# Kernel optimization log

Hardware: AMD Instinct MI355X
Metric: run time of the kernel (lower is better)

## Reference

```python
import jax, jax.numpy as jnp
import numpy as np

NUM_NODES = 100000
NUM_EDGES = 3_200_000
WALKS_PER_NODE = 4
WALK_LENGTH = 8
SKIP_FIRST = True


def setup_inputs() -> dict:
    key = jax.random.key(0)
    k1, k2, k3 = jax.random.split(key, 3)
    edge_index = jax.random.randint(k1, (2, NUM_EDGES), 0, NUM_NODES, dtype=jnp.int32)
    edge_weight = jax.random.uniform(k2, (NUM_EDGES,), dtype=jnp.float32)
    # one uniform per walker per step; S = NUM_NODES * WALKS_PER_NODE
    rand_unif = jax.random.uniform(k3, (NUM_NODES * WALKS_PER_NODE, WALK_LENGTH), dtype=jnp.float32)
    return {"edge_index": edge_index, "edge_weight": edge_weight, "rand_unif": rand_unif}


def _random_walk_edges(edge_index, rand_unif):
    """Returns added [2, S*L] edges (root -> walked node), int dtype."""
    row, col = edge_index[0], edge_index[1]
    # is_sorted=False path: sort edges by source to build CSR
    order = jnp.argsort(row)
    row_s = row[order]
    col_s = col[order]
    deg = jax.ops.segment_sum(jnp.ones_like(row_s), row_s, num_segments=NUM_NODES)  # [N]
    rowptr = jnp.concatenate([jnp.zeros((1,), deg.dtype), jnp.cumsum(deg)])  # [N+1]
    # start = all nodes, repeated walks_per_node times
    start = jnp.tile(jnp.arange(NUM_NODES, dtype=row.dtype), WALKS_PER_NODE)  # [S]

    def step(cur, u):
        d = deg[cur]  # [S]
        off = jnp.minimum((u * d.astype(u.dtype)).astype(cur.dtype), jnp.maximum(d - 1, 0))
        nxt = jnp.where(d > 0, col_s[rowptr[cur] + off], cur)  # stay if isolated
        return nxt, nxt

    _, walks = jax.lax.scan(step, start, rand_unif.T)  # [L_total, S]
    walks = walks.T  # [S, WALK_LENGTH] == n_id[:, 1:]
    k = 1 if SKIP_FIRST else 0  # skip_first drops the first-hop node (n_id[:, 2:])
    targets = walks[:, k:]  # [S, L]
    L = targets.shape[1]
    roots = jnp.broadcast_to(start[:, None], (start.shape[0], L))
    return jnp.stack([roots.reshape(-1), targets.reshape(-1)])  # [2, S*L]


def reference(edge_index, edge_weight, rand_unif):
    added = _random_walk_edges(edge_index, rand_unif)
    out_edge_index = jnp.concatenate([edge_index, added], axis=1)
    added_w = jnp.ones((added.shape[1],), edge_weight.dtype)
    out_edge_weight = jnp.concatenate([edge_weight, added_w])
    return out_edge_index, out_edge_weight
```

## Files before the change

### kernel.cpp

```cpp
#include <hip/hip_runtime.h>

#define ARW_N_NODES   100000
#define ARW_N_EDGES   3200000
#define ARW_N_WALKERS 400000
#define ARW_WLEN      8
#define ARW_LOUT      7
#define ARW_ROW_LEN   6000000
#define ARW_OUT_ELEMS 18000000

#define ARW_NB    196
#define ARW_NT    3125
#define ARW_TP    3136
#define ARW_TILE  1024

#define ARW_HT    0
#define ARW_BT    700000
#define ARW_TOT   1350000
#define ARW_CB    1360000
#define ARW_DEG   1400000
#define ARW_RP    1500000
#define ARW_P     6000000
#define ARW_COLS  12000000

__global__ void AddRandomWalkEdge_16896401342869_kernel() {}

__global__ __launch_bounds__(1024) void arw16896_thist(const int* __restrict__ row,
                                                       int* __restrict__ s) {
    __shared__ int h[256];
    int tid = threadIdx.x;
    if (tid < 256) h[tid] = 0;
    __syncthreads();
    atomicAdd(&h[row[blockIdx.x * ARW_TILE + tid] >> 9], 1);
    __syncthreads();
    if (tid < ARW_NB) s[ARW_HT + tid * ARW_TP + blockIdx.x] = h[tid];
}

__global__ __launch_bounds__(1024) void arw16896_btot(int* __restrict__ s) {
    __shared__ int wsum[16];
    int b = blockIdx.x, tid = threadIdx.x, lane = tid & 63, wid = tid >> 6;
    int acc = 0;
    for (int t = tid; t < ARW_NT; t += 1024) acc += s[ARW_HT + b * ARW_TP + t];
    #pragma unroll
    for (int off = 32; off > 0; off >>= 1) acc += __shfl_down(acc, off, 64);
    if (lane == 0) wsum[wid] = acc;
    __syncthreads();
    if (tid == 0) {
        int a = 0;
        #pragma unroll
        for (int w = 0; w < 16; w++) a += wsum[w];
        s[ARW_TOT + b] = a;
    }
}

__global__ __launch_bounds__(256) void arw16896_bbase(int* __restrict__ s) {
    __shared__ int sm[256];
    int tid = threadIdx.x;
    int v = (tid < ARW_NB) ? s[ARW_TOT + tid] : 0;
    sm[tid] = v;
    __syncthreads();
    for (int off = 1; off < 256; off <<= 1) {
        int x = 0;
        if (tid >= off) x = sm[tid - off];
        __syncthreads();
        sm[tid] += x;
        __syncthreads();
    }
    if (tid < ARW_NB) s[ARW_CB + tid] = sm[tid] - v;
}

__global__ __launch_bounds__(1024) void arw16896_bscan2(int* __restrict__ s) {
    __shared__ int wsum[16];
    int b = blockIdx.x, tid = threadIdx.x, lane = tid & 63, wid = tid >> 6;
    int carry = s[ARW_CB + b];
    for (int c0 = 0; c0 < ARW_NT; c0 += 1024) {
        int t = c0 + tid;
        int v = (t < ARW_NT) ? s[ARW_HT + b * ARW_TP + t] : 0;
        int sv = v;
        #pragma unroll
        for (int off = 1; off < 64; off <<= 1) {
            int x = __shfl_up(sv, off, 64);
            if (lane >= off) sv += x;
        }
        if (lane == 63) wsum[wid] = sv;
        __syncthreads();
        int pre = 0, tot = 0;
        #pragma unroll
        for (int w = 0; w < 16; w++) {
            int x = wsum[w];
            if (w < wid) pre += x;
            tot += x;
        }
        if (t < ARW_NT) s[ARW_BT + b * ARW_TP + t] = carry + pre + sv - v;
        carry += tot;
        __syncthreads();
    }
}

__global__ __launch_bounds__(1024) void arw16896_part(const int* __restrict__ row,
                                                      const int* __restrict__ col,
                                                      int* __restrict__ s) {
    __shared__ unsigned W[16 * 256];
    int tid  = threadIdx.x;
    int wave = tid >> 6, lane = tid & 63;
    int e = blockIdx.x * ARW_TILE + tid;
    int r = row[e], cv = col[e];
    int b = r >> 9;
    W[tid] = 0; W[tid + 1024] = 0; W[tid + 2048] = 0; W[tid + 3072] = 0;
    __syncthreads();
    unsigned long long mask = ~0ULL;
    #pragma unroll
    for (int bit = 0; bit < 8; bit++) {
        unsigned long long bal = __ballot((b >> bit) & 1);
        mask &= ((b >> bit) & 1) ? bal : ~bal;
    }
    int rankw = __popcll(mask & ((1ULL << lane) - 1ULL));
    W[wave * 256 + b] = (unsigned)__popcll(mask);
    __syncthreads();
    int cross = 0;
    for (int w2 = 0; w2 < 16; w2++) {
        if (w2 >= wave) break;
        cross += (int)W[w2 * 256 + b];
    }
    int base = s[ARW_BT + b * ARW_TP + blockIdx.x];
    s[ARW_P + base + cross + rankw] = ((r & 511) << 17) | cv;
}

__global__ __launch_bounds__(1024) void arw16896_pass2(int* __restrict__ s) {
    __shared__ unsigned W[16 * 512];
    __shared__ int hist[512], pref[512], runc[512];
    int tid = threadIdx.x, lane = tid & 63, wave = tid >> 6;
    int b = blockIdx.x;
    int start = s[ARW_BT + b * ARW_TP];
    int end   = (b == ARW_NB - 1) ? ARW_N_EDGES : s[ARW_BT + (b + 1) * ARW_TP];
    int cnt = end - start;
    int rows0 = b << 9;
    int nrows = ARW_N_NODES - rows0; if (nrows > 512) nrows = 512;

    if (tid < 512) hist[tid] = 0;
    __syncthreads();
    for (int k = tid; k < cnt; k += 1024)
        atomicAdd(&hist[(unsigned)s[ARW_P + start + k] >> 17], 1);
    __syncthreads();
    if (tid < 512) pref[tid] = hist[tid];
    __syncthreads();
    for (int off = 1; off < 512; off <<= 1) {
        int x = 0;
        if (tid < 512 && tid >= off) x = pref[tid - off];
        __syncthreads();
        if (tid < 512) pref[tid] += x;
        __syncthreads();
    }
    if (tid < 512) runc[tid] = 0;
    if (tid < nrows) {
        s[ARW_DEG + rows0 + tid] = hist[tid];
        s[ARW_RP  + rows0 + tid] = start + pref[tid] - hist[tid];
    }
    __syncthreads();

    for (int c0 = 0; c0 < cnt; c0 += 1024) {
        int k = c0 + tid;
        int valid = (k < cnt) ? 1 : 0;
        unsigned p = valid ? (unsigned)s[ARW_P + start + k] : 0u;
        unsigned lr = p >> 17;
        #pragma unroll
        for (int j = 0; j < 8; j++) W[tid + j * 1024] = 0;
        __syncthreads();
        unsigned long long mask = ~0ULL;
        #pragma unroll
        for (int bit = 0; bit < 9; bit++) {
            unsigned long long bal = __ballot((lr >> bit) & 1u);
            mask &= ((lr >> bit) & 1u) ? bal : ~bal;
        }
        mask &= __ballot(valid);
        int rankw = __popcll(mask & ((1ULL << lane) - 1ULL));
        if (valid) W[wave * 512 + lr] = (unsigned)__popcll(mask);
        __syncthreads();
        if (valid) {
            int cross = 0;
            for (int w2 = 0; w2 < 16; w2++) {
                if (w2 >= wave) break;
                cross += (int)W[w2 * 512 + lr];
            }
            int pos = start + (pref[lr] - hist[lr]) + runc[lr] + cross + rankw;
            s[ARW_COLS + pos] = (int)(p & 0x1FFFFu);
        }
        __syncthreads();
        if (tid < 512) {
            int a = 0;
            #pragma unroll
            for (int w = 0; w < 16; w++) a += (int)W[w * 512 + tid];
            runc[tid] += a;
        }
        __syncthreads();
    }
}

__global__ __launch_bounds__(256) void arw16896_walk(const float* __restrict__ ru,
                                                     const int* __restrict__ s,
                                                     float* __restrict__ o) {
    __shared__ float tg[256 * ARW_LOUT];
    int tid = threadIdx.x;
    int w = blockIdx.x * 256 + tid;
    if (w < ARW_N_WALKERS) {
        const float4* rp = (const float4*)(ru + (size_t)w * 8);
        float4 ra = rp[0], rb = rp[1];
        float uu[8] = {ra.x, ra.y, ra.z, ra.w, rb.x, rb.y, rb.z, rb.w};
        int cur = w % ARW_N_NODES;
        #pragma unroll
        for (int t = 0; t < ARW_WLEN; t++) {
            int d = s[ARW_DEG + cur];
            if (d > 0) {
                int off = (int)(uu[t] * (float)d);
                if (off > d - 1) off = d - 1;
                cur = s[ARW_COLS + s[ARW_RP + cur] + off];
            }
            if (t >= 1) tg[tid * ARW_LOUT + (t - 1)] = (float)cur;
        }
    }
    __syncthreads();
    int blkW = ARW_N_WALKERS - blockIdx.x * 256;
    if (blkW > 256) blkW = 256;
    int valid = blkW * ARW_LOUT;
    int base = ARW_ROW_LEN + ARW_N_EDGES + blockIdx.x * 256 * ARW_LOUT;
    for (int j = tid; j < valid; j += 256) o[base + j] = tg[j];
}

__global__ __launch_bounds__(256) void arw16896_asm(const int* __restrict__ ei,
                                                    const float* __restrict__ wgt,
                                                    float* __restrict__ o) {
    int i4 = blockIdx.x * blockDim.x + threadIdx.x;
    if (i4 < ARW_N_EDGES / 4) {
        int4 r0 = ((const int4*)ei)[i4];
        int4 r1 = ((const int4*)(ei + ARW_N_EDGES))[i4];
        float4 wv = ((const float4*)wgt)[i4];
        ((float4*)o)[i4] = make_float4((float)r0.x, (float)r0.y, (float)r0.z, (float)r0.w);
        ((float4*)(o + ARW_ROW_LEN))[i4] =
            make_float4((float)r1.x, (float)r1.y, (float)r1.z, (float)r1.w);
        ((float4*)(o + 2 * ARW_ROW_LEN))[i4] = wv;
    }
    if (i4 < (ARW_N_WALKERS * ARW_LOUT) / 4) {
        int i = i4 * 4;
        float4 r;
        r.x = (float)(((i    ) / ARW_LOUT) % ARW_N_NODES);
        r.y = (float)(((i + 1) / ARW_LOUT) % ARW_N_NODES);
        r.z = (float)(((i + 2) / ARW_LOUT) % ARW_N_NODES);
        r.w = (float)(((i + 3) / ARW_LOUT) % ARW_N_NODES);
        ((float4*)(o + ARW_N_EDGES))[i4] = r;
        ((float4*)(o + 2 * ARW_ROW_LEN + ARW_N_EDGES))[i4] = make_float4(1.f, 1.f, 1.f, 1.f);
    }
}

extern "C" void kernel_launch(void* const* d_in, const int* in_sizes, int n_in,
                              void* d_out, int out_size, void* d_ws, size_t ws_size,
                              hipStream_t stream) {
    const int*   ei  = (const int*)d_in[0];
    const float* wgt = (const float*)d_in[1];
    const float* ru  = (const float*)d_in[2];
    int*   s = (int*)d_out;
    float* o = (float*)d_out;
    const int* row = ei;
    const int* col = ei + ARW_N_EDGES;

    arw16896_thist <<<ARW_NT, 1024, 0, stream>>>(row, s);
    arw16896_btot  <<<ARW_NB, 1024, 0, stream>>>(s);
    arw16896_bbase <<<1, 256, 0, stream>>>(s);
    arw16896_bscan2<<<ARW_NB, 1024, 0, stream>>>(s);
    arw16896_part  <<<ARW_NT, 1024, 0, stream>>>(row, col, s);
    arw16896_pass2 <<<ARW_NB, 1024, 0, stream>>>(s);
    arw16896_walk  <<<(ARW_N_WALKERS + 255) / 256, 256, 0, stream>>>(ru, s, o);
    arw16896_asm   <<<(ARW_N_EDGES / 4 + 255) / 256, 256, 0, stream>>>(ei, wgt, o);
}
```

Baseline: 267.0 us.

## Pack rowptr and degree into one word and walk four walkers per thread

Rowptr and degree are packed into a single 32-bit word (22 bits pointer, 10 bits degree), so each walk step does one dependent load instead of two. Each thread now handles the four walkers that share a start node, reusing one load of the start node's packed entry for the first hop. The four independent gather chains are interleaved to expose more memory-level parallelism. The packing assumes degree below 1024 and offsets below about 4M, which holds for these input sizes but is not general. The launch uses a quarter as many threads.

```diff
diff --git a/kernel.cpp b/kernel.cpp
--- a/kernel.cpp
+++ b/kernel.cpp
@@ -17,8 +17,7 @@
 #define ARW_BT    700000
 #define ARW_TOT   1350000
 #define ARW_CB    1360000
-#define ARW_DEG   1400000
-#define ARW_RP    1500000
+#define ARW_PD    1400000
 #define ARW_P     6000000
 #define ARW_COLS  12000000
 
@@ -152,8 +151,9 @@
     }
     if (tid < 512) runc[tid] = 0;
     if (tid < nrows) {
-        s[ARW_DEG + rows0 + tid] = hist[tid];
-        s[ARW_RP  + rows0 + tid] = start + pref[tid] - hist[tid];
+        unsigned deg = (unsigned)hist[tid];
+        unsigned rp  = (unsigned)(start + pref[tid] - hist[tid]);
+        s[ARW_PD + rows0 + tid] = (int)((rp << 10) | deg);
     }
     __syncthreads();
 
@@ -198,31 +198,56 @@
 __global__ __launch_bounds__(256) void arw16896_walk(const float* __restrict__ ru,
                                                      const int* __restrict__ s,
                                                      float* __restrict__ o) {
-    __shared__ float tg[256 * ARW_LOUT];
+    __shared__ float tg[4 * 256 * ARW_LOUT];
     int tid = threadIdx.x;
-    int w = blockIdx.x * 256 + tid;
-    if (w < ARW_N_WALKERS) {
-        const float4* rp = (const float4*)(ru + (size_t)w * 8);
-        float4 ra = rp[0], rb = rp[1];
-        float uu[8] = {ra.x, ra.y, ra.z, ra.w, rb.x, rb.y, rb.z, rb.w};
-        int cur = w % ARW_N_NODES;
-        #pragma unroll
-        for (int t = 0; t < ARW_WLEN; t++) {
-            int d = s[ARW_DEG + cur];
-            if (d > 0) {
-                int off = (int)(uu[t] * (float)d);
+    int v = blockIdx.x * 256 + tid;
+    if (v < ARW_N_NODES) {
+        float uu[4][8];
+        int cur[4];
+        #pragma unroll
+        for (int k = 0; k < 4; k++) {
+            const float4* rp4 = (const float4*)(ru + (size_t)(v + k * ARW_N_NODES) * 8);
+            float4 ra = rp4[0], rb = rp4[1];
+            uu[k][0] = ra.x; uu[k][1] = ra.y; uu[k][2] = ra.z; uu[k][3] = ra.w;
+            uu[k][4] = rb.x; uu[k][5] = rb.y; uu[k][6] = rb.z; uu[k][7] = rb.w;
+        }
+        unsigned pd0 = (unsigned)s[ARW_PD + v];
+        int d0  = (int)(pd0 & 1023u);
+        int rp0 = (int)(pd0 >> 10);
+        #pragma unroll
+        for (int k = 0; k < 4; k++) {
+            int off = (int)(uu[k][0] * (float)d0);
+            if (off > d0 - 1) off = d0 - 1;
+            int nxt = s[ARW_COLS + rp0 + off];
+            cur[k] = (d0 > 0) ? nxt : v;
+        }
+        #pragma unroll
+        for (int t = 1; t < ARW_WLEN; t++) {
+            unsigned pdk[4];
+            #pragma unroll
+            for (int k = 0; k < 4; k++) pdk[k] = (unsigned)s[ARW_PD + cur[k]];
+            #pragma unroll
+            for (int k = 0; k < 4; k++) {
+                int d = (int)(pdk[k] & 1023u);
+                int off = (int)(uu[k][t] * (float)d);
                 if (off > d - 1) off = d - 1;
-                cur = s[ARW_COLS + s[ARW_RP + cur] + off];
+                int nxt = s[ARW_COLS + (int)(pdk[k] >> 10) + off];
+                cur[k] = (d > 0) ? nxt : cur[k];
+                tg[k * (256 * ARW_LOUT) + tid * ARW_LOUT + (t - 1)] = (float)cur[k];
             }
-            if (t >= 1) tg[tid * ARW_LOUT + (t - 1)] = (float)cur;
-        }
-    }
-    __syncthreads();
-    int blkW = ARW_N_WALKERS - blockIdx.x * 256;
-    if (blkW > 256) blkW = 256;
-    int valid = blkW * ARW_LOUT;
-    int base = ARW_ROW_LEN + ARW_N_EDGES + blockIdx.x * 256 * ARW_LOUT;
-    for (int j = tid; j < valid; j += 256) o[base + j] = tg[j];
+        }
+    }
+    __syncthreads();
+    int blkN = ARW_N_NODES - blockIdx.x * 256;
+    if (blkN > 256) blkN = 256;
+    int valid = blkN * ARW_LOUT;
+    #pragma unroll
+    for (int k = 0; k < 4; k++) {
+        int base = ARW_ROW_LEN + ARW_N_EDGES +
+                   (k * ARW_N_NODES + blockIdx.x * 256) * ARW_LOUT;
+        for (int j = tid; j < valid; j += 256)
+            o[base + j] = tg[k * (256 * ARW_LOUT) + j];
+    }
 }
 
 __global__ __launch_bounds__(256) void arw16896_asm(const int* __restrict__ ei,
@@ -267,6 +292,6 @@
     arw16896_bscan2<<<ARW_NB, 1024, 0, stream>>>(s);
     arw16896_part  <<<ARW_NT, 1024, 0, stream>>>(row, col, s);
     arw16896_pass2 <<<ARW_NB, 1024, 0, stream>>>(s);
-    arw16896_walk  <<<(ARW_N_WALKERS + 255) / 256, 256, 0, stream>>>(ru, s, o);
+    arw16896_walk  <<<(ARW_N_NODES + 255) / 256, 256, 0, stream>>>(ru, s, o);
     arw16896_asm   <<<(ARW_N_EDGES / 4 + 255) / 256, 256, 0, stream>>>(ei, wgt, o);
 }
```

Result: faster. 247.2 us (-7.4%).
